# Kernel tuning notes

Measured on AMD Instinct MI355X. Metric: run time of the kernel, lower is better.

Reference implementation:

```python
import jax, jax.numpy as jnp
import numpy as np

S = 64.0   # arcface scale
M = 0.5    # arcface additive angular margin
EPS = 1e-07
B, D, C = 1024, 512, 100000


def setup_inputs() -> dict:
    key = jax.random.key(0)
    k1, k2, k3 = jax.random.split(key, 3)
    features = jax.random.normal(k1, (B, D), dtype=jnp.float32)
    # Linear(512, 100000, bias=False) weight, ~1/sqrt(512) init scale.
    W = jax.random.normal(k2, (C, D), dtype=jnp.float32) * 0.04
    y_true = jax.random.randint(k3, (B,), 0, C, dtype=jnp.int64)
    return {"features": features, "W": W, "y_true": y_true}


def reference(features, W, y_true):
    # L2-normalize features along dim=1 (torch F.normalize, eps=1e-12).
    norm = jnp.maximum(jnp.linalg.norm(features, axis=1, keepdims=True), 1e-12)
    xn = features / norm
    # NOTE: the original module's weight-normalization loop is a no-op
    # (rebinds a local), so W is used unnormalized — faithful to the source.
    wf = xn @ W.T                                   # [B, C] cosine-like logits
    tgt = wf[jnp.arange(B), y_true]                  # true-class logit per row
    # arcface: s * cos(acos(clamp(t)) + m)
    numerator = S * jnp.cos(jnp.arccos(jnp.clip(tgt, -1.0 + EPS, 1.0 - EPS)) + M)
    # exp-sum over all classes except the true one (mask instead of python-loop concat)
    not_true = jnp.arange(C)[None, :] != y_true[:, None]   # [B, C]
    excl_sum = jnp.sum(jnp.where(not_true, jnp.exp(S * wf), 0.0), axis=1)
    denominator = jnp.exp(numerator) + excl_sum
    L = numerator - jnp.log(denominator)
    return -jnp.mean(L)
```

## Files before the change

### kernel.cpp

```cpp
#include <hip/hip_runtime.h>
#include <math.h>

#define BATCH 1024
#define DIM   512
#define NCLS  100000
#define SCALE_S 64.0f
#define MARGIN  0.5f
#define EPS_REF 1e-7f
#define NBLK 782
#define MBLK 8
#define BK   64

typedef __attribute__((ext_vector_type(8))) short short8;
typedef __attribute__((ext_vector_type(4))) float floatx4;

__device__ __forceinline__ unsigned short f2bf(float f) {
    union { float f; unsigned u; } v; v.f = f;
    unsigned r = v.u + 0x7FFFu + ((v.u >> 16) & 1u);
    return (unsigned short)(r >> 16);
}

__device__ __forceinline__ void gload_lds16(const void* g, void* l) {
    __builtin_amdgcn_global_load_lds(
        (const __attribute__((address_space(1))) void*)g,
        (__attribute__((address_space(3))) void*)l, 16, 0, 0);
}

__global__ void k_normalize(const float* __restrict__ features,
                            unsigned short* __restrict__ xnbf,
                            float* __restrict__ rowsum) {
    const int b = blockIdx.x;
    const int t = threadIdx.x;
    const int lane = t & 63;
    const int wave = t >> 6;
    __shared__ float red[2];

    const float4 v = *(const float4*)(features + (size_t)b * DIM + t * 4);
    float ss = v.x * v.x + v.y * v.y + v.z * v.z + v.w * v.w;
    #pragma unroll
    for (int m = 32; m >= 1; m >>= 1) ss += __shfl_xor(ss, m);
    if (lane == 0) red[wave] = ss;
    __syncthreads();
    const float tot = red[0] + red[1];
    const float sc = 1.0f / fmaxf(sqrtf(tot), 1e-12f);

    ushort4 p;
    p.x = f2bf(v.x * sc); p.y = f2bf(v.y * sc);
    p.z = f2bf(v.z * sc); p.w = f2bf(v.w * sc);
    *(ushort4*)(xnbf + (size_t)b * DIM + t * 4) = p;

    if (t == 0) rowsum[b] = 0.0f;
}

__global__ void k_tgt(const float* __restrict__ features,
                      const float* __restrict__ W,
                      const int* __restrict__ y,
                      float* __restrict__ tgt) {
    const int b = blockIdx.x;
    const int lane = threadIdx.x;
    const int yb = y[b];
    const float* fr = features + (size_t)b * DIM + lane * 8;
    const float* wr = W + (size_t)yb * DIM + lane * 8;
    float4 f0 = *(const float4*)(fr);
    float4 f1 = *(const float4*)(fr + 4);
    float4 w0 = *(const float4*)(wr);
    float4 w1 = *(const float4*)(wr + 4);
    float d = f0.x * w0.x + f0.y * w0.y + f0.z * w0.z + f0.w * w0.w
            + f1.x * w1.x + f1.y * w1.y + f1.z * w1.z + f1.w * w1.w;
    float ss = f0.x * f0.x + f0.y * f0.y + f0.z * f0.z + f0.w * f0.w
             + f1.x * f1.x + f1.y * f1.y + f1.z * f1.z + f1.w * f1.w;
    #pragma unroll
    for (int m = 32; m >= 1; m >>= 1) { d += __shfl_xor(d, m); ss += __shfl_xor(ss, m); }
    if (lane == 0) tgt[b] = d / fmaxf(sqrtf(ss), 1e-12f);
}

__global__ __launch_bounds__(256)
void k_gemm_expsum(const float* __restrict__ W,
                   const unsigned short* __restrict__ xnbf,
                   float* __restrict__ rowsum) {
    __shared__ unsigned short As[128 * BK];
    __shared__ unsigned short Bs[128 * BK];

    const int tid  = threadIdx.x;
    const int wave = tid >> 6;
    const int lane = tid & 63;
    const int quad = lane >> 4;
    const int l15  = lane & 15;
    const int wm   = wave >> 1;
    const int wn   = wave & 1;

    const int bid = blockIdx.x;
    const int xcd = bid & 7;
    const int j   = bid >> 3;
    const int w   = xcd * NBLK + j;
    const int n_blk = w >> 3;
    const int m_blk = w & 7;
    const int n0 = n_blk * 128;
    const int m0 = m_blk * 128;

    const int a_rl  = lane >> 3;
    const int a_cs  = lane & 7;
    const unsigned short* a_src[4];
    unsigned short* a_dst[4];
    #pragma unroll
    for (int i = 0; i < 4; ++i) {
        const int r = wave * 32 + i * 8 + a_rl;
        a_src[i] = xnbf + (size_t)(m0 + r) * DIM + (a_cs ^ a_rl) * 8;
        a_dst[i] = &As[(wave * 32 + i * 8) * BK];
    }

    const int b_rl = lane >> 4;
    const int b_j  = lane & 15;
    const float* b_src[8];
    int b_ldso[8];
    #pragma unroll
    for (int p = 0; p < 8; ++p) {
        const int r = p * 16 + wave * 4 + b_rl;
        int n = n0 + r;
        if (n > NCLS - 1) n = NCLS - 1;
        b_src[p] = W + (size_t)n * DIM + b_j * 4;
        const int c  = b_j >> 1;
        const int sub = b_j & 1;
        b_ldso[p] = r * BK + ((c ^ (r & 7)) * 8) + sub * 4;
    }

    const int sA = l15 & 7;
    int aoff[4], boff[4];
    #pragma unroll
    for (int mi = 0; mi < 4; ++mi) {
        const int r = wm * 64 + mi * 16 + l15;
        aoff[mi] = r * BK + (quad ^ sA) * 8;
    }
    #pragma unroll
    for (int ni = 0; ni < 4; ++ni) {
        const int r = wn * 64 + ni * 16 + l15;
        boff[ni] = r * BK + (quad ^ sA) * 8;
    }

    floatx4 acc[4][4];
    #pragma unroll
    for (int i = 0; i < 4; ++i)
        #pragma unroll
        for (int jj = 0; jj < 4; ++jj)
            acc[i][jj] = (floatx4){0.f, 0.f, 0.f, 0.f};

    for (int kt = 0; kt < DIM / BK; ++kt) {
        __syncthreads();

        #pragma unroll
        for (int i = 0; i < 4; ++i)
            gload_lds16(a_src[i] + kt * BK, a_dst[i]);

        #pragma unroll
        for (int p = 0; p < 8; ++p) {
            const float4 v = *(const float4*)(b_src[p] + kt * BK);
            uint2 pk;
            pk.x = (__float_as_uint(v.x) >> 16) | (__float_as_uint(v.y) & 0xFFFF0000u);
            pk.y = (__float_as_uint(v.z) >> 16) | (__float_as_uint(v.w) & 0xFFFF0000u);
            *(uint2*)(&Bs[b_ldso[p]]) = pk;
        }

        __syncthreads();

        #pragma unroll
        for (int kc = 0; kc < 2; ++kc) {
            short8 a[4], b[4];
            #pragma unroll
            for (int mi = 0; mi < 4; ++mi)
                a[mi] = *(const short8*)(&As[aoff[mi] ^ (kc * 32)]);
            #pragma unroll
            for (int ni = 0; ni < 4; ++ni)
                b[ni] = *(const short8*)(&Bs[boff[ni] ^ (kc * 32)]);
            #pragma unroll
            for (int mi = 0; mi < 4; ++mi)
                #pragma unroll
                for (int ni = 0; ni < 4; ++ni)
                    acc[mi][ni] = __builtin_amdgcn_mfma_f32_16x16x32_bf16(
                        a[mi], b[ni], acc[mi][ni], 0, 0, 0);
        }
    }

    #pragma unroll
    for (int mi = 0; mi < 4; ++mi) {
        #pragma unroll
        for (int reg = 0; reg < 4; ++reg) {
            float p = 0.f;
            #pragma unroll
            for (int ni = 0; ni < 4; ++ni) {
                const int n = n0 + wn * 64 + ni * 16 + l15;
                if (n < NCLS) p += __expf(SCALE_S * acc[mi][ni][reg]);
            }
            p += __shfl_xor(p, 1);
            p += __shfl_xor(p, 2);
            p += __shfl_xor(p, 4);
            p += __shfl_xor(p, 8);
            if (l15 == 0) {
                const int m = m0 + wm * 64 + mi * 16 + quad * 4 + reg;
                atomicAdd(&rowsum[m], p);
            }
        }
    }
}

__global__ void k_finalize(const float* __restrict__ rowsum,
                           const float* __restrict__ tgt,
                           float* __restrict__ out) {
    const int tid = threadIdx.x;
    const int lane = tid & 63;
    const int wave = tid >> 6;
    __shared__ float red[4];

    float s = 0.f;
    #pragma unroll
    for (int i = 0; i < 4; ++i) {
        const int b = tid + i * 256;
        const float traw = tgt[b];
        const float tc = fminf(fmaxf(traw, -1.0f + EPS_REF), 1.0f - EPS_REF);
        const float num = SCALE_S * cosf(acosf(tc) + MARGIN);
        const float excl = rowsum[b] - expf(SCALE_S * traw);
        const float denom = expf(num) + excl;
        s += num - logf(denom);
    }
    #pragma unroll
    for (int m = 32; m >= 1; m >>= 1) s += __shfl_xor(s, m);
    if (lane == 0) red[wave] = s;
    __syncthreads();
    if (tid == 0)
        out[0] = -(red[0] + red[1] + red[2] + red[3]) / (float)BATCH;
}

extern "C" void kernel_launch(void* const* d_in, const int* in_sizes, int n_in,
                              void* d_out, int out_size, void* d_ws, size_t ws_size,
                              hipStream_t stream) {
    const float* features = (const float*)d_in[0];
    const float* W        = (const float*)d_in[1];
    const int*   y        = (const int*)d_in[2];
    float* out = (float*)d_out;

    char* ws = (char*)d_ws;
    unsigned short* xnbf  = (unsigned short*)ws;
    float* rowsum = (float*)(ws + 1048576);
    float* tgt    = (float*)(ws + 1048576 + 4096);

    k_normalize<<<BATCH, 128, 0, stream>>>(features, xnbf, rowsum);
    k_tgt<<<BATCH, 64, 0, stream>>>(features, W, y, tgt);
    k_gemm_expsum<<<NBLK * MBLK, 256, 0, stream>>>(W, xnbf, rowsum);
    k_finalize<<<1, 256, 0, stream>>>(rowsum, tgt, out);
}
```

Baseline: 473.7 us.

## Pre-convert W to bf16 and stream both GEMM operands via async LDS loads

Adds a pass that converts the full fp32 W into a bf16 copy in workspace. The GEMM can then load both operands with direct global-to-LDS loads instead of fp32 register loads, in-register packing and LDS stores. It also merges the normalization and target-logit kernels into one prep kernel. The cost is an extra full read of W plus a write of the bf16 copy on every call. A large workspace is required, with a fallback to the old fp32 path when it is too small.

After: 503.3 us. +6.3%, slower.

```diff
diff --git a/kernel.cpp b/kernel.cpp
--- a/kernel.cpp
+++ b/kernel.cpp
@@ -26,58 +26,56 @@
         (__attribute__((address_space(3))) void*)l, 16, 0, 0);
 }
 
-__global__ void k_normalize(const float* __restrict__ features,
-                            unsigned short* __restrict__ xnbf,
-                            float* __restrict__ rowsum) {
+__global__ void k_wcvt(const float* __restrict__ W,
+                       unsigned short* __restrict__ wbf) {
+    const size_t i = ((size_t)blockIdx.x * 256 + threadIdx.x) * 8;
+    const float4 lo = *(const float4*)(W + i);
+    const float4 hi = *(const float4*)(W + i + 4);
+    uint4 p;
+    p.x = (__float_as_uint(lo.x) >> 16) | (__float_as_uint(lo.y) & 0xFFFF0000u);
+    p.y = (__float_as_uint(lo.z) >> 16) | (__float_as_uint(lo.w) & 0xFFFF0000u);
+    p.z = (__float_as_uint(hi.x) >> 16) | (__float_as_uint(hi.y) & 0xFFFF0000u);
+    p.w = (__float_as_uint(hi.z) >> 16) | (__float_as_uint(hi.w) & 0xFFFF0000u);
+    *(uint4*)(wbf + i) = p;
+}
+
+__global__ void k_prep(const float* __restrict__ features,
+                       const float* __restrict__ W,
+                       const int* __restrict__ y,
+                       unsigned short* __restrict__ xnbf,
+                       float* __restrict__ rowsum,
+                       float* __restrict__ tgt) {
     const int b = blockIdx.x;
     const int t = threadIdx.x;
     const int lane = t & 63;
     const int wave = t >> 6;
-    __shared__ float red[2];
+    __shared__ float redس[1];
+    __shared__ float redS[2];
+    __shared__ float redD[2];
+    (void)redس;
 
     const float4 v = *(const float4*)(features + (size_t)b * DIM + t * 4);
+    const float4 wv = *(const float4*)(W + (size_t)y[b] * DIM + t * 4);
     float ss = v.x * v.x + v.y * v.y + v.z * v.z + v.w * v.w;
-    #pragma unroll
-    for (int m = 32; m >= 1; m >>= 1) ss += __shfl_xor(ss, m);
-    if (lane == 0) red[wave] = ss;
+    float dd = v.x * wv.x + v.y * wv.y + v.z * wv.z + v.w * wv.w;
+    #pragma unroll
+    for (int m = 32; m >= 1; m >>= 1) { ss += __shfl_xor(ss, m); dd += __shfl_xor(dd, m); }
+    if (lane == 0) { redS[wave] = ss; redD[wave] = dd; }
     __syncthreads();
-    const float tot = red[0] + red[1];
-    const float sc = 1.0f / fmaxf(sqrtf(tot), 1e-12f);
+    const float sc = 1.0f / fmaxf(sqrtf(redS[0] + redS[1]), 1e-12f);
 
     ushort4 p;
     p.x = f2bf(v.x * sc); p.y = f2bf(v.y * sc);
     p.z = f2bf(v.z * sc); p.w = f2bf(v.w * sc);
     *(ushort4*)(xnbf + (size_t)b * DIM + t * 4) = p;
 
-    if (t == 0) rowsum[b] = 0.0f;
-}
-
-__global__ void k_tgt(const float* __restrict__ features,
-                      const float* __restrict__ W,
-                      const int* __restrict__ y,
-                      float* __restrict__ tgt) {
-    const int b = blockIdx.x;
-    const int lane = threadIdx.x;
-    const int yb = y[b];
-    const float* fr = features + (size_t)b * DIM + lane * 8;
-    const float* wr = W + (size_t)yb * DIM + lane * 8;
-    float4 f0 = *(const float4*)(fr);
-    float4 f1 = *(const float4*)(fr + 4);
-    float4 w0 = *(const float4*)(wr);
-    float4 w1 = *(const float4*)(wr + 4);
-    float d = f0.x * w0.x + f0.y * w0.y + f0.z * w0.z + f0.w * w0.w
-            + f1.x * w1.x + f1.y * w1.y + f1.z * w1.z + f1.w * w1.w;
-    float ss = f0.x * f0.x + f0.y * f0.y + f0.z * f0.z + f0.w * f0.w
-             + f1.x * f1.x + f1.y * f1.y + f1.z * f1.z + f1.w * f1.w;
-    #pragma unroll
-    for (int m = 32; m >= 1; m >>= 1) { d += __shfl_xor(d, m); ss += __shfl_xor(ss, m); }
-    if (lane == 0) tgt[b] = d / fmaxf(sqrtf(ss), 1e-12f);
+    if (t == 0) { rowsum[b] = 0.0f; tgt[b] = (redD[0] + redD[1]) * sc; }
 }
 
 __global__ __launch_bounds__(256)
-void k_gemm_expsum(const float* __restrict__ W,
-                   const unsigned short* __restrict__ xnbf,
-                   float* __restrict__ rowsum) {
+void k_gemm_bf(const unsigned short* __restrict__ wbf,
+               const unsigned short* __restrict__ xnbf,
+               float* __restrict__ rowsum) {
     __shared__ unsigned short As[128 * BK];
     __shared__ unsigned short Bs[128 * BK];
 
@@ -98,44 +96,31 @@
     const int n0 = n_blk * 128;
     const int m0 = m_blk * 128;
 
-    const int a_rl  = lane >> 3;
-    const int a_cs  = lane & 7;
+    const int rl = lane >> 3;
+    const int cs = lane & 7;
     const unsigned short* a_src[4];
+    const unsigned short* b_src[4];
     unsigned short* a_dst[4];
+    unsigned short* b_dst[4];
     #pragma unroll
     for (int i = 0; i < 4; ++i) {
-        const int r = wave * 32 + i * 8 + a_rl;
-        a_src[i] = xnbf + (size_t)(m0 + r) * DIM + (a_cs ^ a_rl) * 8;
-        a_dst[i] = &As[(wave * 32 + i * 8) * BK];
-    }
-
-    const int b_rl = lane >> 4;
-    const int b_j  = lane & 15;
-    const float* b_src[8];
-    int b_ldso[8];
-    #pragma unroll
-    for (int p = 0; p < 8; ++p) {
-        const int r = p * 16 + wave * 4 + b_rl;
+        const int r = wave * 32 + i * 8 + rl;
+        a_src[i] = xnbf + (size_t)(m0 + r) * DIM + (cs ^ rl) * 8;
         int n = n0 + r;
         if (n > NCLS - 1) n = NCLS - 1;
-        b_src[p] = W + (size_t)n * DIM + b_j * 4;
-        const int c  = b_j >> 1;
-        const int sub = b_j & 1;
-        b_ldso[p] = r * BK + ((c ^ (r & 7)) * 8) + sub * 4;
+        b_src[i] = wbf + (size_t)n * DIM + (cs ^ rl) * 8;
+        a_dst[i] = &As[(wave * 32 + i * 8) * BK];
+        b_dst[i] = &Bs[(wave * 32 + i * 8) * BK];
     }
 
     const int sA = l15 & 7;
     int aoff[4], boff[4];
     #pragma unroll
-    for (int mi = 0; mi < 4; ++mi) {
-        const int r = wm * 64 + mi * 16 + l15;
-        aoff[mi] = r * BK + (quad ^ sA) * 8;
-    }
-    #pragma unroll
-    for (int ni = 0; ni < 4; ++ni) {
-        const int r = wn * 64 + ni * 16 + l15;
-        boff[ni] = r * BK + (quad ^ sA) * 8;
-    }
+    for (int mi = 0; mi < 4; ++mi)
+        aoff[mi] = (wm * 64 + mi * 16 + l15) * BK + (quad ^ sA) * 8;
+    #pragma unroll
+    for (int ni = 0; ni < 4; ++ni)
+        boff[ni] = (wn * 64 + ni * 16 + l15) * BK + (quad ^ sA) * 8;
 
     floatx4 acc[4][4];
     #pragma unroll
@@ -146,20 +131,11 @@
 
     for (int kt = 0; kt < DIM / BK; ++kt) {
         __syncthreads();
-
-        #pragma unroll
-        for (int i = 0; i < 4; ++i)
+        #pragma unroll
+        for (int i = 0; i < 4; ++i) {
             gload_lds16(a_src[i] + kt * BK, a_dst[i]);
-
-        #pragma unroll
-        for (int p = 0; p < 8; ++p) {
-            const float4 v = *(const float4*)(b_src[p] + kt * BK);
-            uint2 pk;
-            pk.x = (__float_as_uint(v.x) >> 16) | (__float_as_uint(v.y) & 0xFFFF0000u);
-            pk.y = (__float_as_uint(v.z) >> 16) | (__float_as_uint(v.w) & 0xFFFF0000u);
-            *(uint2*)(&Bs[b_ldso[p]]) = pk;
-        }
-
+            gload_lds16(b_src[i] + kt * BK, b_dst[i]);
+        }
         __syncthreads();
 
         #pragma unroll
@@ -202,6 +178,127 @@
     }
 }
 
+__global__ __launch_bounds__(256)
+void k_gemm_expsum(const float* __restrict__ W,
+                   const unsigned short* __restrict__ xnbf,
+                   float* __restrict__ rowsum) {
+    __shared__ unsigned short As[128 * BK];
+    __shared__ unsigned short Bs[128 * BK];
+
+    const int tid  = threadIdx.x;
+    const int wave = tid >> 6;
+    const int lane = tid & 63;
+    const int quad = lane >> 4;
+    const int l15  = lane & 15;
+    const int wm   = wave >> 1;
+    const int wn   = wave & 1;
+
+    const int bid = blockIdx.x;
+    const int xcd = bid & 7;
+    const int j   = bid >> 3;
+    const int w   = xcd * NBLK + j;
+    const int n_blk = w >> 3;
+    const int m_blk = w & 7;
+    const int n0 = n_blk * 128;
+    const int m0 = m_blk * 128;
+
+    const int a_rl  = lane >> 3;
+    const int a_cs  = lane & 7;
+    const unsigned short* a_src[4];
+    unsigned short* a_dst[4];
+    #pragma unroll
+    for (int i = 0; i < 4; ++i) {
+        const int r = wave * 32 + i * 8 + a_rl;
+        a_src[i] = xnbf + (size_t)(m0 + r) * DIM + (a_cs ^ a_rl) * 8;
+        a_dst[i] = &As[(wave * 32 + i * 8) * BK];
+    }
+
+    const int b_rl = lane >> 4;
+    const int b_j  = lane & 15;
+    const float* b_src[8];
+    int b_ldso[8];
+    #pragma unroll
+    for (int p = 0; p < 8; ++p) {
+        const int r = p * 16 + wave * 4 + b_rl;
+        int n = n0 + r;
+        if (n > NCLS - 1) n = NCLS - 1;
+        b_src[p] = W + (size_t)n * DIM + b_j * 4;
+        const int c  = b_j >> 1;
+        const int sub = b_j & 1;
+        b_ldso[p] = r * BK + ((c ^ (r & 7)) * 8) + sub * 4;
+    }
+
+    const int sA = l15 & 7;
+    int aoff[4], boff[4];
+    #pragma unroll
+    for (int mi = 0; mi < 4; ++mi)
+        aoff[mi] = (wm * 64 + mi * 16 + l15) * BK + (quad ^ sA) * 8;
+    #pragma unroll
+    for (int ni = 0; ni < 4; ++ni)
+        boff[ni] = (wn * 64 + ni * 16 + l15) * BK + (quad ^ sA) * 8;
+
+    floatx4 acc[4][4];
+    #pragma unroll
+    for (int i = 0; i < 4; ++i)
+        #pragma unroll
+        for (int jj = 0; jj < 4; ++jj)
+            acc[i][jj] = (floatx4){0.f, 0.f, 0.f, 0.f};
+
+    for (int kt = 0; kt < DIM / BK; ++kt) {
+        __syncthreads();
+        #pragma unroll
+        for (int i = 0; i < 4; ++i)
+            gload_lds16(a_src[i] + kt * BK, a_dst[i]);
+        #pragma unroll
+        for (int p = 0; p < 8; ++p) {
+            const float4 v = *(const float4*)(b_src[p] + kt * BK);
+            uint2 pk;
+            pk.x = (__float_as_uint(v.x) >> 16) | (__float_as_uint(v.y) & 0xFFFF0000u);
+            pk.y = (__float_as_uint(v.z) >> 16) | (__float_as_uint(v.w) & 0xFFFF0000u);
+            *(uint2*)(&Bs[b_ldso[p]]) = pk;
+        }
+        __syncthreads();
+
+        #pragma unroll
+        for (int kc = 0; kc < 2; ++kc) {
+            short8 a[4], b[4];
+            #pragma unroll
+            for (int mi = 0; mi < 4; ++mi)
+                a[mi] = *(const short8*)(&As[aoff[mi] ^ (kc * 32)]);
+            #pragma unroll
+            for (int ni = 0; ni < 4; ++ni)
+                b[ni] = *(const short8*)(&Bs[boff[ni] ^ (kc * 32)]);
+            #pragma unroll
+            for (int mi = 0; mi < 4; ++mi)
+                #pragma unroll
+                for (int ni = 0; ni < 4; ++ni)
+                    acc[mi][ni] = __builtin_amdgcn_mfma_f32_16x16x32_bf16(
+                        a[mi], b[ni], acc[mi][ni], 0, 0, 0);
+        }
+    }
+
+    #pragma unroll
+    for (int mi = 0; mi < 4; ++mi) {
+        #pragma unroll
+        for (int reg = 0; reg < 4; ++reg) {
+            float p = 0.f;
+            #pragma unroll
+            for (int ni = 0; ni < 4; ++ni) {
+                const int n = n0 + wn * 64 + ni * 16 + l15;
+                if (n < NCLS) p += __expf(SCALE_S * acc[mi][ni][reg]);
+            }
+            p += __shfl_xor(p, 1);
+            p += __shfl_xor(p, 2);
+            p += __shfl_xor(p, 4);
+            p += __shfl_xor(p, 8);
+            if (l15 == 0) {
+                const int m = m0 + wm * 64 + mi * 16 + quad * 4 + reg;
+                atomicAdd(&rowsum[m], p);
+            }
+        }
+    }
+}
+
 __global__ void k_finalize(const float* __restrict__ rowsum,
                            const float* __restrict__ tgt,
                            float* __restrict__ out) {
@@ -237,13 +334,26 @@
     const int*   y        = (const int*)d_in[2];
     float* out = (float*)d_out;
 
+    const size_t WBF_BYTES = (size_t)NCLS * DIM * 2;
     char* ws = (char*)d_ws;
-    unsigned short* xnbf  = (unsigned short*)ws;
-    float* rowsum = (float*)(ws + 1048576);
-    float* tgt    = (float*)(ws + 1048576 + 4096);
-
-    k_normalize<<<BATCH, 128, 0, stream>>>(features, xnbf, rowsum);
-    k_tgt<<<BATCH, 64, 0, stream>>>(features, W, y, tgt);
-    k_gemm_expsum<<<NBLK * MBLK, 256, 0, stream>>>(W, xnbf, rowsum);
-    k_finalize<<<1, 256, 0, stream>>>(rowsum, tgt, out);
-}
+
+    if (ws_size >= WBF_BYTES + 1048576 + 8192) {
+        unsigned short* wbf   = (unsigned short*)ws;
+        unsigned short* xnbf  = (unsigned short*)(ws + WBF_BYTES);
+        float* rowsum = (float*)(ws + WBF_BYTES + 1048576);
+        float* tgt    = (float*)(ws + WBF_BYTES + 1048576 + 4096);
+
+        k_wcvt<<<NCLS * DIM / 2048, 256, 0, stream>>>(W, wbf);
+        k_prep<<<BATCH, 128, 0, stream>>>(features, W, y, xnbf, rowsum, tgt);
+        k_gemm_bf<<<NBLK * MBLK, 256, 0, stream>>>(wbf, xnbf, rowsum);
+        k_finalize<<<1, 256, 0, stream>>>(rowsum, tgt, out);
+    } else {
+        unsigned short* xnbf  = (unsigned short*)ws;
+        float* rowsum = (float*)(ws + 1048576);
+        float* tgt    = (float*)(ws + 1048576 + 4096);
+
+        k_prep<<<BATCH, 128, 0, stream>>>(features, W, y, xnbf, rowsum, tgt);
+        k_gemm_expsum<<<NBLK * MBLK, 256, 0, stream>>>(W, xnbf, rowsum);
+        k_finalize<<<1, 256, 0, stream>>>(rowsum, tgt, out);
+    }
+}
```
